# Performance work log

Measured on AMD Instinct MI355X. Metric: run time of the kernel, lower is better.

## Reference

```python
import jax, jax.numpy as jnp
import numpy as np


def setup_inputs() -> dict:
    key0 = jax.random.key(0)
    kq, kk, kv = jax.random.split(key0, 3)
    B, S, E = 4, 2048, 1024
    query = jax.random.normal(kq, (B, S, E), dtype=jnp.float32)
    key = jax.random.normal(kk, (B, S, E), dtype=jnp.float32)
    value = jax.random.normal(kv, (B, S, E), dtype=jnp.float32)
    attn_mask = jnp.zeros((B, S, S), dtype=jnp.float32)
    return {"query": query, "key": key, "value": value, "attn_mask": attn_mask}


def reference(query, key, value, attn_mask):
    # qk = Q K^T / sqrt(E) + mask; softmax over last dim; dropout is
    # identity in eval mode (reference baseline); out = attn @ V.
    E = query.shape[-1]
    scale = 1.0 / jnp.sqrt(jnp.asarray(E, dtype=query.dtype))
    qk = jnp.einsum("bqe,bke->bqk", query, key) * scale + attn_mask
    attn = jax.nn.softmax(qk, axis=-1)
    out = jnp.einsum("bqk,bke->bqe", attn, value)
    return out
```

## Files before the change

kernel.cpp:

```cpp
#include <hip/hip_runtime.h>
#include <stdint.h>
#include <math.h>

typedef unsigned short u16;
typedef short bf16x8 __attribute__((ext_vector_type(8)));
typedef unsigned short u16x8 __attribute__((ext_vector_type(8)));
typedef unsigned short u16x4 __attribute__((ext_vector_type(4)));
typedef float f32x4 __attribute__((ext_vector_type(4)));

typedef __attribute__((address_space(1))) const void gvoid;
typedef __attribute__((address_space(3))) void lvoid;

#define LOG2E 1.4426950408889634f

__device__ __forceinline__ float bf2f(u16 u) {
  union { unsigned int i; float f; } v; v.i = ((unsigned int)u) << 16; return v.f;
}
__device__ __forceinline__ u16 f2bf(float f) {
  union { float ff; unsigned int i; } v; v.ff = f;
  unsigned int x = v.i;
  return (u16)((x + 0x7FFFu + ((x >> 16) & 1u)) >> 16);
}

__global__ __launch_bounds__(256)
void cvt2_f32_bf16(const float* __restrict__ s0, u16* __restrict__ d0,
                   const float* __restrict__ s1, u16* __restrict__ d1, long n)
{
  const long nb = n / 2048;
  const float* src = (blockIdx.x < nb) ? s0 : s1;
  u16* dst         = (blockIdx.x < nb) ? d0 : d1;
  const long bid   = (blockIdx.x < nb) ? blockIdx.x : (blockIdx.x - nb);
  long i = (bid * 256 + threadIdx.x) * 8;
  if (i + 8 > n) return;
  f32x4 a = *(const f32x4*)&src[i];
  f32x4 b = *(const f32x4*)&src[i + 4];
  u16x8 o;
#pragma unroll
  for (int j = 0; j < 4; j++) { o[j] = f2bf(a[j]); o[4 + j] = f2bf(b[j]); }
  *(u16x8*)&dst[i] = o;
}

__global__ __launch_bounds__(256)
void cvt_f32_bf16(const float* __restrict__ src, u16* __restrict__ dst, long n)
{
  long i = ((long)blockIdx.x * 256 + threadIdx.x) * 8;
  if (i + 8 > n) return;
  f32x4 a = *(const f32x4*)&src[i];
  f32x4 b = *(const f32x4*)&src[i + 4];
  u16x8 o;
#pragma unroll
  for (int j = 0; j < 4; j++) { o[j] = f2bf(a[j]); o[4 + j] = f2bf(b[j]); }
  *(u16x8*)&dst[i] = o;
}

__global__ __launch_bounds__(256)
void transcvt_v(const float* __restrict__ V, u16* __restrict__ VT, int S, int E)
{
  __shared__ u16 t[64][72];
  const int b = blockIdx.z;
  const float* Vb = V + (long)b * S * E;
  u16* VTb = VT + (long)b * S * E;
  const int k0 = blockIdx.x * 64, n0 = blockIdx.y * 64;
  const int tid = threadIdx.x;
#pragma unroll
  for (int p = 0; p < 2; p++) {
    int kk = p * 32 + (tid >> 3);
    int nn = (tid & 7) * 8;
    f32x4 a = *(const f32x4*)&Vb[(long)(k0 + kk) * E + n0 + nn];
    f32x4 c = *(const f32x4*)&Vb[(long)(k0 + kk) * E + n0 + nn + 4];
#pragma unroll
    for (int j = 0; j < 4; j++) { t[nn + j][kk] = f2bf(a[j]); t[nn + 4 + j][kk] = f2bf(c[j]); }
  }
  __syncthreads();
#pragma unroll
  for (int p = 0; p < 2; p++) {
    int nn = p * 32 + (tid >> 3);
    int kk = (tid & 7) * 8;
    u16x8 u;
#pragma unroll
    for (int j = 0; j < 8; j++) u[j] = t[nn][kk + j];
    *(u16x8*)&VTb[(long)(n0 + nn) * S + k0 + kk] = u;
  }
}

__global__ __launch_bounds__(512, 1)
void gemm_bt_256(const u16* __restrict__ A, int lda,
                 const u16* __restrict__ B, int ldb, long bBatchStride,
                 u16* __restrict__ C, int ldc,
                 int K, float scale, int S)
{
  __shared__ u16 LA[2][256][64];
  __shared__ u16 LB[2][256][64];

  const int tid  = threadIdx.x;
  const int lane = tid & 63;
  const int wave = tid >> 6;
  const int wm   = wave >> 2;
  const int wn   = wave & 3;
  const long gTile = (long)blockIdx.y * 256;
  const int  bidx  = (int)(gTile / S);
  const int  nTile = blockIdx.x * 256;

  const u16* Ab = A + gTile * (long)lda;
  const u16* Bb = B + (long)bidx * bBatchStride + (long)nTile * ldb;

  const int lm  = lane & 15;
  const int lmx = lm & 7;
  const int l47 = lane >> 4;
  const int srw = lane >> 3;
  const int scg = (((lane & 7) ^ (lane >> 3)) * 8);

  f32x4 acc[8][4];
#pragma unroll
  for (int i = 0; i < 8; i++)
#pragma unroll
    for (int j = 0; j < 4; j++) acc[i][j] = (f32x4){0.f, 0.f, 0.f, 0.f};

  bf16x8 afr[8], bA[4], bB[4];

#define STG_A(buf, T, h)                                                      \
  {                                                                           \
    _Pragma("unroll")                                                         \
    for (int p_ = 0; p_ < 2; p_++) {                                          \
      const int ch_ = wave * 2 + p_;                                          \
      const int rr_ = (h) * 128 + ch_ * 8 + srw;                              \
      __builtin_amdgcn_global_load_lds(                                       \
          (gvoid*)&Ab[(long)rr_ * lda + (T) * 64 + scg],                      \
          (lvoid*)((char*)&LA[0][0][0] + (buf) * 32768 + (h) * 16384 + ch_ * 1024), \
          16, 0, 0);                                                          \
    }                                                                         \
  }
#define STG_B(buf, T, h)                                                      \
  {                                                                           \
    _Pragma("unroll")                                                         \
    for (int p_ = 0; p_ < 2; p_++) {                                          \
      const int ch_ = wave * 2 + p_;                                          \
      const int rr_ = (h) * 128 + ch_ * 8 + srw;                              \
      __builtin_amdgcn_global_load_lds(                                       \
          (gvoid*)&Bb[(long)rr_ * ldb + (T) * 64 + scg],                      \
          (lvoid*)((char*)&LB[0][0][0] + (buf) * 32768 + (h) * 16384 + ch_ * 1024), \
          16, 0, 0);                                                          \
    }                                                                         \
  }

#define LDA_HALF(buf, mh)                                                     \
  {                                                                           \
    _Pragma("unroll")                                                         \
    for (int m_ = 0; m_ < 4; m_++)                                            \
      _Pragma("unroll")                                                       \
      for (int kk_ = 0; kk_ < 2; kk_++)                                       \
        afr[m_ * 2 + kk_] = *(const bf16x8*)&LA[buf][wm * 128 + ((mh) * 4 + m_) * 16 + lm][(((kk_ * 4 + l47) ^ lmx) * 8)]; \
  }
#define LDB_HALF(buf, nh, dst)                                                \
  {                                                                           \
    _Pragma("unroll")                                                         \
    for (int n_ = 0; n_ < 2; n_++)                                            \
      _Pragma("unroll")                                                       \
      for (int kk_ = 0; kk_ < 2; kk_++)                                       \
        dst[n_ * 2 + kk_] = *(const bf16x8*)&LB[buf][wn * 64 + ((nh) * 2 + n_) * 16 + lm][(((kk_ * 4 + l47) ^ lmx) * 8)]; \
  }

#define PH(mh, nh, bp)                                                        \
  {                                                                           \
    __builtin_amdgcn_sched_barrier(0);                                        \
    __builtin_amdgcn_s_barrier();                                             \
    asm volatile("s_waitcnt lgkmcnt(0)" ::: "memory");                        \
    __builtin_amdgcn_sched_barrier(0);                                        \
    __builtin_amdgcn_s_setprio(1);                                            \
    _Pragma("unroll")                                                         \
    for (int m_ = 0; m_ < 4; m_++)                                            \
      _Pragma("unroll")                                                       \
      for (int n_ = 0; n_ < 2; n_++)                                          \
        _Pragma("unroll")                                                     \
        for (int kk_ = 0; kk_ < 2; kk_++)                                     \
          acc[(mh) * 4 + m_][(nh) * 2 + n_] =                                 \
              __builtin_amdgcn_mfma_f32_16x16x32_bf16(                        \
                  afr[m_ * 2 + kk_], bp[n_ * 2 + kk_],                        \
                  acc[(mh) * 4 + m_][(nh) * 2 + n_], 0, 0, 0);                \
    __builtin_amdgcn_s_setprio(0);                                            \
    __builtin_amdgcn_sched_barrier(0);                                        \
    __builtin_amdgcn_s_barrier();                                             \
  }

  const int NT = K >> 6;
  const int NI = NT >> 1;

  STG_A(0, 0, 0); STG_A(0, 0, 1); STG_B(0, 0, 0); STG_B(0, 0, 1);
  STG_A(1, 1, 0); STG_B(1, 1, 0);
  asm volatile("s_waitcnt vmcnt(0)" ::: "memory");
  __builtin_amdgcn_sched_barrier(0);
  __builtin_amdgcn_s_barrier();

  for (int i = 0; i < NI - 1; i++) {
    const int t0 = 2 * i, t1 = t0 + 1;
    LDA_HALF(0, 0); LDB_HALF(0, 0, bA);
    STG_B(1, t1, 1);
    PH(0, 0, bA);
    LDB_HALF(0, 1, bB);
    STG_A(1, t1, 1);
    PH(0, 1, bB);
    LDA_HALF(0, 1);
    STG_A(0, t0 + 2, 0);
    PH(1, 0, bA);
    STG_B(0, t0 + 2, 0);
    asm volatile("s_waitcnt vmcnt(4)" ::: "memory");
    PH(1, 1, bB);
    LDA_HALF(1, 0); LDB_HALF(1, 0, bA);
    STG_B(0, t0 + 2, 1);
    PH(0, 0, bA);
    LDB_HALF(1, 1, bB);
    STG_A(0, t0 + 2, 1);
    PH(0, 1, bB);
    LDA_HALF(1, 1);
    STG_A(1, t1 + 2, 0);
    PH(1, 0, bA);
    STG_B(1, t1 + 2, 0);
    asm volatile("s_waitcnt vmcnt(4)" ::: "memory");
    PH(1, 1, bB);
  }

  {
    const int t1 = NT - 1;
    LDA_HALF(0, 0); LDB_HALF(0, 0, bA);
    STG_B(1, t1, 1);
    PH(0, 0, bA);
    LDB_HALF(0, 1, bB);
    STG_A(1, t1, 1);
    PH(0, 1, bB);
    LDA_HALF(0, 1);
    PH(1, 0, bA);
    asm volatile("s_waitcnt vmcnt(0)" ::: "memory");
    PH(1, 1, bB);
    LDA_HALF(1, 0); LDB_HALF(1, 0, bA);
    PH(0, 0, bA);
    LDB_HALF(1, 1, bB);
    PH(0, 1, bB);
    LDA_HALF(1, 1);
    PH(1, 0, bA);
    PH(1, 1, bB);
  }

  const int lr = (lane >> 4) * 4;
#pragma unroll
  for (int mf = 0; mf < 8; mf++) {
#pragma unroll
    for (int nf = 0; nf < 4; nf++) {
      long gr = gTile + wm * 128 + mf * 16 + lr;
      int  cc = nTile + wn * 64 + nf * 16 + lm;
#pragma unroll
      for (int i2 = 0; i2 < 4; i2++)
        C[(gr + i2) * (long)ldc + cc] = f2bf(acc[mf][nf][i2] * scale);
    }
  }
#undef STG_A
#undef STG_B
#undef LDA_HALF
#undef LDB_HALF
#undef PH
}

template<int HASMASK, int COUT>
__global__ __launch_bounds__(256, 3)
void gemm_bt_fast(const u16* __restrict__ A, int lda, long aRowOff,
                  const u16* __restrict__ B, int ldb, long bBatchStride,
                  void* __restrict__ Cp, int ldc, long cRowOff,
                  const float* __restrict__ maskf,
                  int K, float scale, long g0, int S)
{
  const int tid  = threadIdx.x;
  const int lane = tid & 63;
  const int wave = tid >> 6;
  const long gTile = g0 + (long)blockIdx.y * 128;
  const int  bidx  = (int)(gTile / S);
  const int  nTile = blockIdx.x * 128;

  __shared__ u16 As[128][32];
  __shared__ u16 Bs[128][32];

  const u16* Ab = A + (gTile - aRowOff) * (long)lda;
  const u16* Bb = B + (long)bidx * bBatchStride + (long)nTile * ldb;

  const int qm = (wave >> 1) * 64;
  const int qn = (wave & 1) * 64;
  const int lm  = lane & 15;
  const int lkB = (lane >> 4) * 16;

  const int sr = lane >> 2;
  const int sc = (lane & 3) * 8;

  f32x4 acc[4][4];
#pragma unroll
  for (int i = 0; i < 4; i++)
#pragma unroll
    for (int j = 0; j < 4; j++) acc[i][j] = (f32x4){0.f, 0.f, 0.f, 0.f};

  for (int k0 = 0; k0 < K; k0 += 32) {
#pragma unroll
    for (int p = 0; p < 2; p++) {
      const int chunk = wave * 2 + p;
      const int r = chunk * 16 + sr;
      __builtin_amdgcn_global_load_lds(
          (gvoid*)&Ab[(long)r * lda + k0 + sc],
          (lvoid*)((char*)&As[0][0] + chunk * 1024),
          16, 0, 0);
      __builtin_amdgcn_global_load_lds(
          (gvoid*)&Bb[(long)r * ldb + k0 + sc],
          (lvoid*)((char*)&Bs[0][0] + chunk * 1024),
          16, 0, 0);
    }
    __syncthreads();

    bf16x8 af[4], bfr[4];
#pragma unroll
    for (int rt = 0; rt < 4; rt++)
      af[rt] = *(const bf16x8*)((const char*)&As[qm + rt * 16 + lm][0] + lkB);
#pragma unroll
    for (int ct = 0; ct < 4; ct++)
      bfr[ct] = *(const bf16x8*)((const char*)&Bs[qn + ct * 16 + lm][0] + lkB);

#pragma unroll
    for (int rt = 0; rt < 4; rt++)
#pragma unroll
      for (int ct = 0; ct < 4; ct++)
        acc[rt][ct] = __builtin_amdgcn_mfma_f32_16x16x32_bf16(af[rt], bfr[ct], acc[rt][ct], 0, 0, 0);
    __syncthreads();
  }

  const int lr = (lane >> 4) * 4;
#pragma unroll
  for (int rt = 0; rt < 4; rt++) {
#pragma unroll
    for (int ct = 0; ct < 4; ct++) {
      long gr = gTile + qm + rt * 16 + lr;
      int  cc = nTile + qn + ct * 16 + lm;
#pragma unroll
      for (int i = 0; i < 4; i++) {
        float v = acc[rt][ct][i] * scale;
        if (HASMASK) v += maskf[(gr + i) * (long)ldc + cc];
        if (COUT == 0)
          ((u16*)Cp)[(gr + i - cRowOff) * (long)ldc + cc] = f2bf(v);
        else
          ((float*)Cp)[(gr + i - cRowOff) * (long)ldc + cc] = v;
      }
    }
  }
}

template<int ASRC, int BSRC, int BMODE, int HASMASK, int COUT>
__global__ __launch_bounds__(256, 2)
void gemm_bt(const void* __restrict__ Ap, int lda, long aRowOff,
             const void* __restrict__ Bp, int ldb, long bBatchStride,
             void* __restrict__ Cp, int ldc, long cRowOff,
             const float* __restrict__ maskf,
             int K, float scale, long g0, int S)
{
  const int tid  = threadIdx.x;
  const int lane = tid & 63;
  const int wave = tid >> 6;
  const long gTile = g0 + (long)blockIdx.y * 128;
  const int  b     = (int)(gTile / S);
  const int  nTile = blockIdx.x * 128;

  __shared__ u16 As[128][40];
  __shared__ u16 Bs[128][40];

  const int qm = (wave >> 1) * 64;
  const int qn = (wave & 1) * 64;

  f32x4 acc[4][4];
#pragma unroll
  for (int i = 0; i < 4; i++)
#pragma unroll
    for (int j = 0; j < 4; j++) acc[i][j] = (f32x4){0.f, 0.f, 0.f, 0.f};

  const u16*   Ab = (const u16*)Ap   + (gTile - aRowOff) * (long)lda;
  const float* Af = (const float*)Ap + (gTile - aRowOff) * (long)lda;
  const u16*   Bb = (const u16*)Bp   + (long)b * bBatchStride;
  const float* Bf = (const float*)Bp + (long)b * bBatchStride;

  const int lm = lane & 15;
  const int lk = (lane >> 4) * 8;

  for (int k0 = 0; k0 < K; k0 += 32) {
    if (ASRC == 0) {
      int srow = tid >> 2, scol = (tid & 3) * 8;
#pragma unroll
      for (int p = 0; p < 2; p++) {
        int r = p * 64 + srow;
        *(u16x8*)&As[r][scol] = *(const u16x8*)&Ab[(long)r * lda + k0 + scol];
      }
    } else {
      int srow = tid >> 3, scol = (tid & 7) * 4;
#pragma unroll
      for (int p = 0; p < 4; p++) {
        int r = p * 32 + srow;
        f32x4 a = *(const f32x4*)&Af[(long)r * lda + k0 + scol];
        u16x4 o;
#pragma unroll
        for (int j = 0; j < 4; j++) o[j] = f2bf(a[j]);
        *(u16x4*)&As[r][scol] = o;
      }
    }
    if (BMODE == 0) {
      if (BSRC == 0) {
        int srow = tid >> 2, scol = (tid & 3) * 8;
#pragma unroll
        for (int p = 0; p < 2; p++) {
          int r = p * 64 + srow;
          *(u16x8*)&Bs[r][scol] = *(const u16x8*)&Bb[(long)(nTile + r) * ldb + k0 + scol];
        }
      } else {
        int srow = tid >> 3, scol = (tid & 7) * 4;
#pragma unroll
        for (int p = 0; p < 4; p++) {
          int r = p * 32 + srow;
          f32x4 a = *(const f32x4*)&Bf[(long)(nTile + r) * ldb + k0 + scol];
          u16x4 o;
#pragma unroll
          for (int j = 0; j < 4; j++) o[j] = f2bf(a[j]);
          *(u16x4*)&Bs[r][scol] = o;
        }
      }
    }
    __syncthreads();

    bf16x8 af[4], bfr[4];
#pragma unroll
    for (int rt = 0; rt < 4; rt++)
      af[rt] = *(const bf16x8*)&As[qm + rt * 16 + lm][lk];
    if (BMODE == 0) {
#pragma unroll
      for (int ct = 0; ct < 4; ct++)
        bfr[ct] = *(const bf16x8*)&Bs[qn + ct * 16 + lm][lk];
    } else {
#pragma unroll
      for (int ct = 0; ct < 4; ct++) {
        const float* vp = Bf + (long)(k0 + lk) * ldb + nTile + qn + ct * 16 + lm;
#pragma unroll
        for (int j = 0; j < 8; j++) bfr[ct][j] = (short)f2bf(vp[(long)j * ldb]);
      }
    }
#pragma unroll
    for (int rt = 0; rt < 4; rt++)
#pragma unroll
      for (int ct = 0; ct < 4; ct++)
        acc[rt][ct] = __builtin_amdgcn_mfma_f32_16x16x32_bf16(af[rt], bfr[ct], acc[rt][ct], 0, 0, 0);
    __syncthreads();
  }

  const int lr = (lane >> 4) * 4;
#pragma unroll
  for (int rt = 0; rt < 4; rt++) {
#pragma unroll
    for (int ct = 0; ct < 4; ct++) {
      long gr = gTile + qm + rt * 16 + lr;
      int  cc = nTile + qn + ct * 16 + lm;
#pragma unroll
      for (int i = 0; i < 4; i++) {
        float v = acc[rt][ct][i] * scale;
        if (HASMASK) v += maskf[(gr + i) * (long)ldc + cc];
        if (COUT == 0)
          ((u16*)Cp)[(gr + i - cRowOff) * (long)ldc + cc] = f2bf(v);
        else
          ((float*)Cp)[(gr + i - cRowOff) * (long)ldc + cc] = v;
      }
    }
  }
}

__global__ __launch_bounds__(256)
void softmax_rows_wave(u16* __restrict__ Sbuf, const float* __restrict__ maskf,
                       int ncols)
{
  const int wave = threadIdx.x >> 6;
  const int lane = threadIdx.x & 63;
  const long row = (long)blockIdx.x * 4 + wave;
  u16* rp = Sbuf + row * (long)ncols;
  const float* mp = maskf + row * (long)ncols;

  float x[32];
  float m = -3.0e38f;
#pragma unroll
  for (int j = 0; j < 4; j++) {
    const int c = j * 512 + lane * 8;
    u16x8 u = *(const u16x8*)&rp[c];
    f32x4 ma = *(const f32x4*)&mp[c];
    f32x4 mb = *(const f32x4*)&mp[c + 4];
#pragma unroll
    for (int i = 0; i < 4; i++) {
      x[j * 8 + i]     = bf2f(u[i])     + ma[i];
      x[j * 8 + 4 + i] = bf2f(u[4 + i]) + mb[i];
    }
#pragma unroll
    for (int i = 0; i < 8; i++) m = fmaxf(m, x[j * 8 + i]);
  }
#pragma unroll
  for (int off = 32; off; off >>= 1) m = fmaxf(m, __shfl_xor(m, off, 64));

  float s = 0.f;
#pragma unroll
  for (int i = 0; i < 32; i++) { x[i] = exp2f((x[i] - m) * LOG2E); s += x[i]; }
#pragma unroll
  for (int off = 32; off; off >>= 1) s += __shfl_xor(s, off, 64);
  const float inv = 1.0f / s;

#pragma unroll
  for (int j = 0; j < 4; j++) {
    const int c = j * 512 + lane * 8;
    u16x8 o;
#pragma unroll
    for (int i = 0; i < 8; i++) o[i] = f2bf(x[j * 8 + i] * inv);
    *(u16x8*)&rp[c] = o;
  }
}

template<int HASM>
__global__ __launch_bounds__(256)
void softmax_rows(u16* __restrict__ Sbuf, const float* __restrict__ maskf, int ncols)
{
  const long row = blockIdx.x;
  u16* rp = Sbuf + row * (long)ncols;
  const int tid = threadIdx.x;

  u16x8 u = *(const u16x8*)&rp[tid * 8];
  float x[8];
  if (HASM) {
    const float* mp = maskf + row * (long)ncols + tid * 8;
    f32x4 ma = *(const f32x4*)&mp[0];
    f32x4 mb = *(const f32x4*)&mp[4];
#pragma unroll
    for (int i = 0; i < 4; i++) { x[i] = bf2f(u[i]) + ma[i]; x[4 + i] = bf2f(u[4 + i]) + mb[i]; }
  } else {
#pragma unroll
    for (int i = 0; i < 8; i++) x[i] = bf2f(u[i]);
  }
  float m = -3.0e38f;
#pragma unroll
  for (int i = 0; i < 8; i++) m = fmaxf(m, x[i]);
#pragma unroll
  for (int off = 32; off; off >>= 1) m = fmaxf(m, __shfl_xor(m, off, 64));
  __shared__ float redm[4];
  if ((tid & 63) == 0) redm[tid >> 6] = m;
  __syncthreads();
  m = fmaxf(fmaxf(redm[0], redm[1]), fmaxf(redm[2], redm[3]));

  float e[8];
  float s = 0.f;
#pragma unroll
  for (int i = 0; i < 8; i++) { e[i] = exp2f((x[i] - m) * LOG2E); s += e[i]; }
#pragma unroll
  for (int off = 32; off; off >>= 1) s += __shfl_xor(s, off, 64);
  __shared__ float reds[4];
  if ((tid & 63) == 0) reds[tid >> 6] = s;
  __syncthreads();
  s = reds[0] + reds[1] + reds[2] + reds[3];

  float inv = 1.0f / s;
  u16x8 o;
#pragma unroll
  for (int i = 0; i < 8; i++) o[i] = f2bf(e[i] * inv);
  *(u16x8*)&rp[tid * 8] = o;
}

extern "C" void kernel_launch(void* const* d_in, const int* in_sizes, int n_in,
                              void* d_out, int out_size, void* d_ws, size_t ws_size,
                              hipStream_t stream)
{
  const float* Q    = (const float*)d_in[0];
  const float* Km   = (const float*)d_in[1];
  const float* V    = (const float*)d_in[2];
  const float* mask = (const float*)d_in[3];
  float* out = (float*)d_out;

  const long qsz = in_sizes[0];
  const long msz = in_sizes[3];
  const long E = 1024;
  const long S = (msz / qsz) * E;
  const long B = qsz / (S * E);
  const long G = B * S;
  const float scale = 1.0f / sqrtf((float)E);

  const size_t mergedBytes = (size_t)(2 * qsz) * 2 + (size_t)G * S * 2;
  if (ws_size >= mergedBytes && (S % 512) == 0 && (G % 256) == 0) {
    char* w = (char*)d_ws;
    u16* Qb   = (u16*)w;
    u16* Kb   = (u16*)(w + (size_t)qsz * 2);
    u16* Sbuf = (u16*)(w + (size_t)(2 * qsz) * 2);
    u16* VTb  = Qb;

    cvt2_f32_bf16<<<dim3((unsigned)(2 * qsz / 2048)), 256, 0, stream>>>(
        Q, Qb, Km, Kb, qsz);

    gemm_bt_256<<<dim3(S / 256, G / 256), 512, 0, stream>>>(
        Qb, (int)E, Kb, (int)E, S * E,
        Sbuf, (int)S, (int)E, scale, (int)S);

    softmax_rows_wave<<<dim3((unsigned)(G / 4)), 256, 0, stream>>>(
        Sbuf, mask, (int)S);

    transcvt_v<<<dim3(S / 64, E / 64, B), 256, 0, stream>>>(V, VTb, (int)S, (int)E);

    gemm_bt_fast<0, 1><<<dim3(E / 128, G / 128), 256, 0, stream>>>(
        Sbuf, (int)S, 0L, VTb, (int)S, E * S,
        out, (int)E, 0L, nullptr, (int)S, 1.0f, 0L, (int)S);
    return;
  }

  const size_t convBytes = (size_t)(3 * qsz) * 2;
  const size_t rowBytes  = (size_t)S * 2;
  char* w = (char*)d_ws;
  size_t avail = ws_size;
  const bool haveConv = (ws_size >= convBytes + 128 * rowBytes);

  u16 *Qb = nullptr, *Kb = nullptr, *VTb = nullptr;
  if (haveConv) {
    Qb  = (u16*)w;              w += (size_t)qsz * 2;
    Kb  = (u16*)w;              w += (size_t)qsz * 2;
    VTb = (u16*)w;              w += (size_t)qsz * 2;
    avail -= convBytes;
  }
  long Rmax = (long)((avail / rowBytes) / 128) * 128;
  if (Rmax > G) Rmax = G;
  if (Rmax < 128) Rmax = 128;
  u16* Sbuf = (u16*)w;

  if (haveConv) {
    cvt_f32_bf16<<<dim3((unsigned)(qsz / 2048)), 256, 0, stream>>>(Q, Qb, qsz);
    cvt_f32_bf16<<<dim3((unsigned)(qsz / 2048)), 256, 0, stream>>>(Km, Kb, qsz);
    transcvt_v<<<dim3(S / 64, E / 64, B), 256, 0, stream>>>(V, VTb, (int)S, (int)E);
  }

  for (long g0 = 0; g0 < G; g0 += Rmax) {
    const long R = (G - g0 < Rmax) ? (G - g0) : Rmax;
    if (haveConv) {
      gemm_bt_fast<1, 0><<<dim3(S / 128, R / 128), 256, 0, stream>>>(
          Qb, (int)E, 0L, Kb, (int)E, S * E,
          Sbuf, (int)S, g0, mask, (int)E, scale, g0, (int)S);
    } else {
      gemm_bt<1, 1, 0, 1, 0><<<dim3(S / 128, R / 128), 256, 0, stream>>>(
          Q, (int)E, 0L, Km, (int)E, S * E,
          Sbuf, (int)S, g0, mask, (int)E, scale, g0, (int)S);
    }
    softmax_rows<0><<<dim3(R), 256, 0, stream>>>(Sbuf, nullptr, (int)S);
    if (haveConv) {
      gemm_bt_fast<0, 1><<<dim3(E / 128, R / 128), 256, 0, stream>>>(
          Sbuf, (int)S, g0, VTb, (int)S, E * S,
          out, (int)E, 0L, nullptr, (int)S, 1.0f, g0, (int)S);
    } else {
      gemm_bt<0, 1, 1, 0, 1><<<dim3(E / 128, R / 128), 256, 0, stream>>>(
          Sbuf, (int)S, g0, V, (int)E, S * E,
          out, (int)E, 0L, nullptr, (int)S, 1.0f, g0, (int)S);
    }
  }
}
```

Baseline: 277.6 us.

## Add 256x128 double-buffered P@V GEMM kernel with direct-to-LDS loads

Replaces the generic 128x128 gemm_bt_fast used for the attention-times-V product with a dedicated 512-thread kernel computing 256x128 output tiles. It stages A and B into LDS with global_load_lds, double-buffers them and interleaves MFMA phases with the loads, mirroring the existing QK^T 256 kernel. The larger tile is meant to increase operand reuse and cut global traffic for the P@V GEMM. The cost is fewer blocks (E/128 x G/256 = 256), about one per CU, with occupancy limited to one block.

```diff
diff --git a/kernel.cpp b/kernel.cpp
--- a/kernel.cpp
+++ b/kernel.cpp
@@ -142,7 +142,6 @@
           16, 0, 0);                                                          \
     }                                                                         \
   }
-
 #define LDA_HALF(buf, mh)                                                     \
   {                                                                           \
     _Pragma("unroll")                                                         \
@@ -159,7 +158,6 @@
       for (int kk_ = 0; kk_ < 2; kk_++)                                       \
         dst[n_ * 2 + kk_] = *(const bf16x8*)&LB[buf][wn * 64 + ((nh) * 2 + n_) * 16 + lm][(((kk_ * 4 + l47) ^ lmx) * 8)]; \
   }
-
 #define PH(mh, nh, bp)                                                        \
   {                                                                           \
     __builtin_amdgcn_sched_barrier(0);                                        \
@@ -259,6 +257,176 @@
 #undef PH
 }
 
+__global__ __launch_bounds__(512, 1)
+void gemm_pv_256(const u16* __restrict__ A, int lda,
+                 const u16* __restrict__ B, int ldb, long bBatchStride,
+                 float* __restrict__ C, int ldc,
+                 int K, int S)
+{
+  __shared__ u16 LA[2][256][64];
+  __shared__ u16 LB[2][128][64];
+
+  const int tid  = threadIdx.x;
+  const int lane = tid & 63;
+  const int wave = tid >> 6;
+  const int wm   = wave >> 1;
+  const int wn   = wave & 1;
+  const long gTile = (long)blockIdx.y * 256;
+  const int  bidx  = (int)(gTile / S);
+  const int  nTile = blockIdx.x * 128;
+
+  const u16* Ab = A + gTile * (long)lda;
+  const u16* Bb = B + (long)bidx * bBatchStride + (long)nTile * ldb;
+
+  const int lm  = lane & 15;
+  const int lmx = lm & 7;
+  const int l47 = lane >> 4;
+  const int srw = lane >> 3;
+  const int scg = (((lane & 7) ^ (lane >> 3)) * 8);
+
+  f32x4 acc[4][4];
+#pragma unroll
+  for (int i = 0; i < 4; i++)
+#pragma unroll
+    for (int j = 0; j < 4; j++) acc[i][j] = (f32x4){0.f, 0.f, 0.f, 0.f};
+
+  bf16x8 afr[4], bA[4], bB[4];
+
+#define STG_A(buf, T, h)                                                      \
+  {                                                                           \
+    _Pragma("unroll")                                                         \
+    for (int p_ = 0; p_ < 2; p_++) {                                          \
+      const int ch_ = wave * 2 + p_;                                          \
+      const int rr_ = (h) * 128 + ch_ * 8 + srw;                              \
+      __builtin_amdgcn_global_load_lds(                                       \
+          (gvoid*)&Ab[(long)rr_ * lda + (T) * 64 + scg],                      \
+          (lvoid*)((char*)&LA[0][0][0] + (buf) * 32768 + (h) * 16384 + ch_ * 1024), \
+          16, 0, 0);                                                          \
+    }                                                                         \
+  }
+#define STG_B(buf, T, h)                                                      \
+  {                                                                           \
+    const int rr_ = (h) * 64 + wave * 8 + srw;                                \
+    __builtin_amdgcn_global_load_lds(                                         \
+        (gvoid*)&Bb[(long)rr_ * ldb + (T) * 64 + scg],                        \
+        (lvoid*)((char*)&LB[0][0][0] + (buf) * 16384 + (h) * 8192 + wave * 1024), \
+        16, 0, 0);                                                            \
+  }
+#define LDA_HALF(buf, mh)                                                     \
+  {                                                                           \
+    _Pragma("unroll")                                                         \
+    for (int m_ = 0; m_ < 2; m_++)                                            \
+      _Pragma("unroll")                                                       \
+      for (int kk_ = 0; kk_ < 2; kk_++)                                       \
+        afr[m_ * 2 + kk_] = *(const bf16x8*)&LA[buf][wm * 64 + ((mh) * 2 + m_) * 16 + lm][(((kk_ * 4 + l47) ^ lmx) * 8)]; \
+  }
+#define LDB_HALF(buf, nh, dst)                                                \
+  {                                                                           \
+    _Pragma("unroll")                                                         \
+    for (int n_ = 0; n_ < 2; n_++)                                            \
+      _Pragma("unroll")                                                       \
+      for (int kk_ = 0; kk_ < 2; kk_++)                                       \
+        dst[n_ * 2 + kk_] = *(const bf16x8*)&LB[buf][wn * 64 + ((nh) * 2 + n_) * 16 + lm][(((kk_ * 4 + l47) ^ lmx) * 8)]; \
+  }
+#define PH(mh, nh, bp)                                                        \
+  {                                                                           \
+    __builtin_amdgcn_sched_barrier(0);                                        \
+    __builtin_amdgcn_s_barrier();                                             \
+    asm volatile("s_waitcnt lgkmcnt(0)" ::: "memory");                        \
+    __builtin_amdgcn_sched_barrier(0);                                        \
+    __builtin_amdgcn_s_setprio(1);                                            \
+    _Pragma("unroll")                                                         \
+    for (int m_ = 0; m_ < 2; m_++)                                            \
+      _Pragma("unroll")                                                       \
+      for (int n_ = 0; n_ < 2; n_++)                                          \
+        _Pragma("unroll")                                                     \
+        for (int kk_ = 0; kk_ < 2; kk_++)                                     \
+          acc[(mh) * 2 + m_][(nh) * 2 + n_] =                                 \
+              __builtin_amdgcn_mfma_f32_16x16x32_bf16(                        \
+                  afr[m_ * 2 + kk_], bp[n_ * 2 + kk_],                        \
+                  acc[(mh) * 2 + m_][(nh) * 2 + n_], 0, 0, 0);                \
+    __builtin_amdgcn_s_setprio(0);                                            \
+    __builtin_amdgcn_sched_barrier(0);                                        \
+    __builtin_amdgcn_s_barrier();                                             \
+  }
+
+  const int NT = K >> 6;
+  const int NI = NT >> 1;
+
+  STG_A(0, 0, 0); STG_A(0, 0, 1); STG_B(0, 0, 0); STG_B(0, 0, 1);
+  STG_A(1, 1, 0); STG_B(1, 1, 0);
+  asm volatile("s_waitcnt vmcnt(0)" ::: "memory");
+  __builtin_amdgcn_sched_barrier(0);
+  __builtin_amdgcn_s_barrier();
+
+  for (int i = 0; i < NI - 1; i++) {
+    const int t0 = 2 * i, t1 = t0 + 1;
+    LDA_HALF(0, 0); LDB_HALF(0, 0, bA);
+    STG_B(1, t1, 1);
+    PH(0, 0, bA);
+    LDB_HALF(0, 1, bB);
+    STG_A(1, t1, 1);
+    PH(0, 1, bB);
+    LDA_HALF(0, 1);
+    STG_A(0, t0 + 2, 0);
+    PH(1, 0, bA);
+    STG_B(0, t0 + 2, 0);
+    asm volatile("s_waitcnt vmcnt(3)" ::: "memory");
+    PH(1, 1, bB);
+    LDA_HALF(1, 0); LDB_HALF(1, 0, bA);
+    STG_B(0, t0 + 2, 1);
+    PH(0, 0, bA);
+    LDB_HALF(1, 1, bB);
+    STG_A(0, t0 + 2, 1);
+    PH(0, 1, bB);
+    LDA_HALF(1, 1);
+    STG_A(1, t1 + 2, 0);
+    PH(1, 0, bA);
+    STG_B(1, t1 + 2, 0);
+    asm volatile("s_waitcnt vmcnt(3)" ::: "memory");
+    PH(1, 1, bB);
+  }
+
+  {
+    const int t1 = NT - 1;
+    LDA_HALF(0, 0); LDB_HALF(0, 0, bA);
+    STG_B(1, t1, 1);
+    PH(0, 0, bA);
+    LDB_HALF(0, 1, bB);
+    STG_A(1, t1, 1);
+    PH(0, 1, bB);
+    LDA_HALF(0, 1);
+    PH(1, 0, bA);
+    asm volatile("s_waitcnt vmcnt(0)" ::: "memory");
+    PH(1, 1, bB);
+    LDA_HALF(1, 0); LDB_HALF(1, 0, bA);
+    PH(0, 0, bA);
+    LDB_HALF(1, 1, bB);
+    PH(0, 1, bB);
+    LDA_HALF(1, 1);
+    PH(1, 0, bA);
+    PH(1, 1, bB);
+  }
+
+  const int lr = (lane >> 4) * 4;
+#pragma unroll
+  for (int mf = 0; mf < 4; mf++) {
+#pragma unroll
+    for (int nf = 0; nf < 4; nf++) {
+      long gr = gTile + wm * 64 + mf * 16 + lr;
+      int  cc = nTile + wn * 64 + nf * 16 + lm;
+#pragma unroll
+      for (int i2 = 0; i2 < 4; i2++)
+        C[(gr + i2) * (long)ldc + cc] = acc[mf][nf][i2];
+    }
+  }
+#undef STG_A
+#undef STG_B
+#undef LDA_HALF
+#undef LDB_HALF
+#undef PH
+}
+
 template<int HASMASK, int COUT>
 __global__ __launch_bounds__(256, 3)
 void gemm_bt_fast(const u16* __restrict__ A, int lda, long aRowOff,
@@ -581,7 +749,7 @@
   const float scale = 1.0f / sqrtf((float)E);
 
   const size_t mergedBytes = (size_t)(2 * qsz) * 2 + (size_t)G * S * 2;
-  if (ws_size >= mergedBytes && (S % 512) == 0 && (G % 256) == 0) {
+  if (ws_size >= mergedBytes && (S % 512) == 0 && (G % 256) == 0 && (E % 128) == 0) {
     char* w = (char*)d_ws;
     u16* Qb   = (u16*)w;
     u16* Kb   = (u16*)(w + (size_t)qsz * 2);
@@ -600,9 +768,9 @@
 
     transcvt_v<<<dim3(S / 64, E / 64, B), 256, 0, stream>>>(V, VTb, (int)S, (int)E);
 
-    gemm_bt_fast<0, 1><<<dim3(E / 128, G / 128), 256, 0, stream>>>(
-        Sbuf, (int)S, 0L, VTb, (int)S, E * S,
-        out, (int)E, 0L, nullptr, (int)S, 1.0f, 0L, (int)S);
+    gemm_pv_256<<<dim3(E / 128, G / 256), 512, 0, stream>>>(
+        Sbuf, (int)S, VTb, (int)S, E * S,
+        out, (int)E, (int)S, (int)S);
     return;
   }
 
```

Result: no change. 278.3 us (+0.3%).
